# Performance work log

Hardware: AMD Instinct MI355X
Metric: run time of the kernel (lower is better)

Reference implementation:

```python
import jax, jax.numpy as jnp
import numpy as np

M_USERS = 100000
N_ITEMS = 50000
NUM_NODES = M_USERS + N_ITEMS
DIM = 64
N_EDGES = 3200000
BATCH = 1024
N_NEGS = 40
REG = 1e-4
NUM_LAYERS = 2


def setup_inputs() -> dict:
    key = jax.random.key(0)
    ks = jax.random.split(key, 14)
    xav = lambda k, shp: jax.random.normal(k, shp, dtype=jnp.float32) * np.float32(np.sqrt(2.0 / (shp[0] + shp[-1])))
    return {
        "E": xav(ks[0], (NUM_NODES, DIM)),
        "E2": xav(ks[1], (NUM_NODES, DIM)),
        "W0": xav(ks[2], (DIM, DIM)),
        "b0": jnp.zeros((DIM,), jnp.float32),
        "W1": xav(ks[3], (DIM, DIM)),
        "b1": jnp.zeros((DIM,), jnp.float32),
        "attn_W": xav(ks[4], (DIM, DIM)),
        "attn_b": jnp.zeros((DIM,), jnp.float32),
        "q_W": xav(ks[5], (1, DIM)),
        "w": jax.random.normal(ks[6], (BATCH,), dtype=jnp.float32),
        "edge_index": jax.random.randint(ks[7], (2, N_EDGES), 0, NUM_NODES, dtype=jnp.int64),
        "u": jax.random.randint(ks[8], (BATCH,), 0, M_USERS, dtype=jnp.int64),
        "v": jax.random.randint(ks[9], (BATCH,), 0, NUM_NODES, dtype=jnp.int64),
        "n": jax.random.randint(ks[10], (BATCH, N_NEGS), 0, NUM_NODES, dtype=jnp.int64),
    }


def _aggregate(E, E2, W0, b0, W1, b1, attn_W, attn_b, q_W, row, col):
    # LightGCN branch: symmetric degree-normalized scatter-add, NUM_LAYERS hops
    deg = jax.ops.segment_sum(jnp.ones_like(col, dtype=E.dtype), col, num_segments=NUM_NODES)
    dinv = jnp.where(deg > 0, jax.lax.rsqrt(jnp.maximum(deg, 1e-12)), 0.0)
    norm = dinv[row] * dinv[col]  # [E]

    def conv(x):
        msg = norm[:, None] * x[row]  # [E, D]
        return jax.ops.segment_sum(msg, col, num_segments=NUM_NODES)

    acc = E
    x = E
    for _ in range(NUM_LAYERS):
        x = conv(x)
        acc = acc + x
    z_p = acc / (NUM_LAYERS + 1)

    # MLP branch (eval mode: dropout disabled)
    h = jax.nn.relu(E2 @ W0.T + b0)
    z_n = jax.nn.relu(h @ W1.T + b1)

    # attention fusion
    w_p = jnp.tanh(z_p @ attn_W.T + attn_b) @ q_W.T  # [NUM_NODES, 1]
    w_n = jnp.tanh(z_n @ attn_W.T + attn_b) @ q_W.T
    alpha = jax.nn.softmax(jnp.concatenate([w_p, w_n], axis=1), axis=1)
    return alpha[:, :1] * z_p + alpha[:, 1:] * z_n


def reference(E, E2, W0, b0, W1, b1, attn_W, attn_b, q_W, w, edge_index, u, v, n):
    row, col = edge_index[0], edge_index[1]
    Z = _aggregate(E, E2, W0, b0, W1, b1, attn_W, attn_b, q_W, row, col)
    u_ = Z[u]            # [B, D]
    v_ = Z[v]            # [B, D]
    n_ = Z[n]            # [B, K, D]
    pos = jnp.sum(u_ * v_, axis=1)                      # [B]
    neg = jnp.einsum('bd,bkd->bk', u_, n_)              # [B, K]
    coef = -0.5 * jnp.sign(w) + 1.5                     # [B]
    sbpr = jax.nn.log_sigmoid(coef[:, None] * pos[:, None] - neg)  # [B, K]
    reg_loss = jnp.sum(u_ ** 2) + jnp.sum(v_ ** 2) + jnp.sum(n_ ** 2)
    return -jnp.sum(sbpr) + REG * reg_loss
```

## Files before the change

### kernel.cpp

```cpp
#include <hip/hip_runtime.h>
#include <hip/hip_fp8.h>
#include <math.h>

#define NUM_NODES 150000
#define DIM 64
#define N_EDGES 3200000
#define BATCH 1024
#define N_NEGS 40
#define REG_COEF 1e-4f

#define BK_BITS 9
#define BK_NODES 512
#define NBK ((NUM_NODES + BK_NODES - 1) >> BK_BITS)
#define TILE 8192
#define NT ((N_EDGES + TILE - 1) / TILE)
#define HSIZE (NBK * NT)
#define SCAN_B 1024
#define NB2 ((HSIZE + SCAN_B - 1) / SCAN_B)
#define NLIST (BATCH * (N_NEGS + 2))

typedef _Float16 half2v __attribute__((ext_vector_type(2)));
typedef _Float16 half4v __attribute__((ext_vector_type(4)));

__global__ __launch_bounds__(256) void histo_kernel(const int* __restrict__ col,
                                                    int* __restrict__ hist) {
    __shared__ int h[NBK];
    int t = threadIdx.x;
    for (int i = t; i < NBK; i += 256) h[i] = 0;
    __syncthreads();
    int e0 = blockIdx.x * TILE;
    int e1 = e0 + TILE; if (e1 > N_EDGES) e1 = N_EDGES;
    for (int i = e0 + t; i < e1; i += 256) atomicAdd(&h[col[i] >> BK_BITS], 1);
    __syncthreads();
    for (int i = t; i < NBK; i += 256) hist[i * NT + blockIdx.x] = h[i];
}

__global__ void scan_partial_kernel(const int* __restrict__ src, int* __restrict__ partial, int n) {
    int t = threadIdx.x;
    int g = blockIdx.x * SCAN_B + t;
    int v = (g < n) ? src[g] : 0;
    for (int m = 1; m < 64; m <<= 1) v += __shfl_xor(v, m);
    __shared__ int ws[16];
    if ((t & 63) == 0) ws[t >> 6] = v;
    __syncthreads();
    if (t < 16) {
        int s = ws[t];
        for (int m = 1; m < 16; m <<= 1) s += __shfl_xor(s, m);
        if (t == 0) partial[blockIdx.x] = s;
    }
}

__global__ void scan_base_kernel(int* __restrict__ partial, int nb, int chunks) {
    int l = threadIdx.x;
    int carry = 0;
    for (int c = 0; c < chunks; c++) {
        int idx = c * 64 + l;
        int v = (idx < nb) ? partial[idx] : 0;
        int inc = v;
        for (int m = 1; m < 64; m <<= 1) {
            int t = __shfl_up(inc, m);
            if (l >= m) inc += t;
        }
        int excl = inc - v + carry;
        if (idx < nb) partial[idx] = excl;
        carry += __shfl(inc, 63);
    }
}

__global__ void scan_apply_kernel(int* __restrict__ data, const int* __restrict__ partial, int n) {
    __shared__ int lds[SCAN_B];
    int t = threadIdx.x;
    int g = blockIdx.x * SCAN_B + t;
    int v = (g < n) ? data[g] : 0;
    int val = v;
    lds[t] = val;
    __syncthreads();
    for (int o = 1; o < SCAN_B; o <<= 1) {
        int add = (t >= o) ? lds[t - o] : 0;
        __syncthreads();
        val += add;
        lds[t] = val;
        __syncthreads();
    }
    if (g < n) data[g] = partial[blockIdx.x] + val - v;
}

__global__ __launch_bounds__(256) void partition_kernel(const int* __restrict__ row,
                                                        const int* __restrict__ col,
                                                        const int* __restrict__ hist,
                                                        unsigned* __restrict__ staging) {
    __shared__ int base[NBK];
    __shared__ int cnt[NBK];
    int t = threadIdx.x;
    for (int i = t; i < NBK; i += 256) { base[i] = hist[i * NT + blockIdx.x]; cnt[i] = 0; }
    __syncthreads();
    int e0 = blockIdx.x * TILE;
    int e1 = e0 + TILE; if (e1 > N_EDGES) e1 = N_EDGES;
    for (int i = e0 + t; i < e1; i += 256) {
        int c = col[i];
        int b = c >> BK_BITS;
        int r = atomicAdd(&cnt[b], 1);
        staging[base[b] + r] = ((unsigned)(c & (BK_NODES - 1)) << 18) | (unsigned)row[i];
    }
}

__global__ __launch_bounds__(512) void fill3_kernel(const int* __restrict__ hist,
                                                    const unsigned* __restrict__ staging,
                                                    const float* __restrict__ E,
                                                    int* __restrict__ off,
                                                    float* __restrict__ dinv,
                                                    float* __restrict__ sq,
                                                    int* __restrict__ csr_row,
                                                    __hip_fp8x4_e4m3* __restrict__ xnE4) {
    __shared__ int cnt[BK_NODES];
    __shared__ int lds[BK_NODES];
    __shared__ float sdinv[BK_NODES];
    int b = blockIdx.x;
    int t = threadIdx.x;
    int node0 = b << BK_BITS;
    int bstart = hist[b * NT];
    int bend = (b + 1 < NBK) ? hist[(b + 1) * NT] : N_EDGES;
    cnt[t] = 0;
    __syncthreads();
    for (int i = bstart + t; i < bend; i += 512) atomicAdd(&cnt[staging[i] >> 18], 1);
    __syncthreads();
    int v = cnt[t];
    int val = v;
    lds[t] = val;
    __syncthreads();
    for (int o = 1; o < BK_NODES; o <<= 1) {
        int add = (t >= o) ? lds[t - o] : 0;
        __syncthreads();
        val += add;
        lds[t] = val;
        __syncthreads();
    }
    int cursor = bstart + val - v;
    int node = node0 + t;
    float dv = (v > 0) ? rsqrtf((float)v) : 0.f;
    if (node < NUM_NODES) {
        off[node] = cursor;
        dinv[node] = dv;
        sq[node] = sqrtf((float)v);
    }
    sdinv[t] = dv;
    cnt[t] = cursor;
    __syncthreads();
    for (int i = bstart + t; i < bend; i += 512) {
        unsigned s = staging[i];
        int pos = atomicAdd(&cnt[s >> 18], 1);
        csr_row[pos] = (int)(s & 0x3FFFFu);
    }
    int nvalid = NUM_NODES - node0; if (nvalid > BK_NODES) nvalid = BK_NODES;
    int groups = nvalid << 4;
    const float4* E4 = (const float4*)E + ((size_t)node0 << 4);
    __hip_fp8x4_e4m3* out4 = xnE4 + ((size_t)node0 << 4);
    for (int gi = t; gi < groups; gi += 512) {
        float4 e = E4[gi];
        float s = 16.f * sdinv[gi >> 4];
        out4[gi] = __hip_fp8x4_e4m3(make_float4(s * e.x, s * e.y, s * e.z, s * e.w));
    }
    if (b == 0 && t == 0) off[NUM_NODES] = N_EDGES;
}

__global__ void flag_kernel(const int* __restrict__ u, const int* __restrict__ v,
                            const int* __restrict__ n, char* __restrict__ flags) {
    int i = blockIdx.x * blockDim.x + threadIdx.x;
    if (i >= NLIST) return;
    int id;
    if (i < BATCH) id = u[i];
    else if (i < 2 * BATCH) id = v[i - BATCH];
    else id = n[i - 2 * BATCH];
    flags[id] = 1;
}

__global__ void compact_kernel(const char* __restrict__ flags, int* __restrict__ list,
                               int* __restrict__ count) {
    int i = blockIdx.x * blockDim.x + threadIdx.x;
    if (i < NUM_NODES && flags[i]) {
        int pos = atomicAdd(count, 1);
        list[pos] = i;
    }
}

__global__ __launch_bounds__(256) void conv1_kernel(const int* __restrict__ off,
                                                    const int* __restrict__ csr_row,
                                                    const float* __restrict__ dinv,
                                                    const __hip_fp8x4_e4m3* __restrict__ xq,
                                                    _Float16* __restrict__ yh) {
    int gid = blockIdx.x * blockDim.x + threadIdx.x;
    int grp = gid >> 4;
    int g = threadIdx.x & 15;
    if (grp >= NUM_NODES) return;
    int start = off[grp];
    int end = off[grp + 1];
    float a0 = 0.f, a1 = 0.f, a2 = 0.f, a3 = 0.f;
    int i = start;
    for (; i + 3 < end; i += 4) {
        int r0 = csr_row[i];
        int r1 = csr_row[i + 1];
        int r2 = csr_row[i + 2];
        int r3 = csr_row[i + 3];
        float4 v0 = static_cast<float4>(xq[((size_t)r0 << 4) + g]);
        float4 v1 = static_cast<float4>(xq[((size_t)r1 << 4) + g]);
        float4 v2 = static_cast<float4>(xq[((size_t)r2 << 4) + g]);
        float4 v3 = static_cast<float4>(xq[((size_t)r3 << 4) + g]);
        a0 += v0.x + v1.x + v2.x + v3.x;
        a1 += v0.y + v1.y + v2.y + v3.y;
        a2 += v0.z + v1.z + v2.z + v3.z;
        a3 += v0.w + v1.w + v2.w + v3.w;
    }
    for (; i < end; ++i) {
        int r = csr_row[i];
        float4 v = static_cast<float4>(xq[((size_t)r << 4) + g]);
        a0 += v.x; a1 += v.y; a2 += v.z; a3 += v.w;
    }
    float dv = dinv[grp];
    float s = dv * dv * (1.f / 16.f);
    union { _Float16 h[4]; short4 s4; } u;
    u.h[0] = (_Float16)(s * a0);
    u.h[1] = (_Float16)(s * a1);
    u.h[2] = (_Float16)(s * a2);
    u.h[3] = (_Float16)(s * a3);
    ((short4*)yh)[((size_t)grp << 4) + g] = u.s4;
}

__global__ __launch_bounds__(256) void conv2_kernel(const int* __restrict__ off,
                                                    const int* __restrict__ csr_row,
                                                    const float* __restrict__ dinv,
                                                    const _Float16* __restrict__ xh,
                                                    float* __restrict__ x2,
                                                    const int* __restrict__ list,
                                                    const int* __restrict__ count) {
    int gid = blockIdx.x * blockDim.x + threadIdx.x;
    int li = gid >> 4;
    int g = threadIdx.x & 15;
    if (li >= *count) return;
    int nd = list[li];
    int start = off[nd];
    int end = off[nd + 1];
    const short4* xh4 = (const short4*)xh;
    float a0 = 0.f, a1 = 0.f, a2 = 0.f, a3 = 0.f;
    int i = start;
    for (; i + 3 < end; i += 4) {
        int r0 = csr_row[i];
        int r1 = csr_row[i + 1];
        int r2 = csr_row[i + 2];
        int r3 = csr_row[i + 3];
        union { short4 s4; _Float16 h[4]; } u0, u1, u2, u3;
        u0.s4 = xh4[((size_t)r0 << 4) + g];
        u1.s4 = xh4[((size_t)r1 << 4) + g];
        u2.s4 = xh4[((size_t)r2 << 4) + g];
        u3.s4 = xh4[((size_t)r3 << 4) + g];
        a0 += (float)u0.h[0] + (float)u1.h[0] + (float)u2.h[0] + (float)u3.h[0];
        a1 += (float)u0.h[1] + (float)u1.h[1] + (float)u2.h[1] + (float)u3.h[1];
        a2 += (float)u0.h[2] + (float)u1.h[2] + (float)u2.h[2] + (float)u3.h[2];
        a3 += (float)u0.h[3] + (float)u1.h[3] + (float)u2.h[3] + (float)u3.h[3];
    }
    for (; i < end; ++i) {
        int r = csr_row[i];
        union { short4 s4; _Float16 h[4]; } u;
        u.s4 = xh4[((size_t)r << 4) + g];
        a0 += (float)u.h[0]; a1 += (float)u.h[1];
        a2 += (float)u.h[2]; a3 += (float)u.h[3];
    }
    float dv = dinv[nd];
    ((float4*)x2)[((size_t)nd << 4) + g] = make_float4(dv * a0, dv * a1, dv * a2, dv * a3);
}

__global__ __launch_bounds__(256, 5) void fuse_kernel(
    const float* __restrict__ E, const float* __restrict__ E2,
    const float* __restrict__ W0, const float* __restrict__ b0,
    const float* __restrict__ W1, const float* __restrict__ b1,
    const float* __restrict__ AW, const float* __restrict__ ab,
    const float* __restrict__ qW,
    const _Float16* __restrict__ xn1, const float* __restrict__ sq,
    const float* x2, float* Z,
    const int* __restrict__ list, const int* __restrict__ count) {
    __shared__ __align__(16) _Float16 W0h[4096];
    __shared__ __align__(16) _Float16 W1h[4096];
    __shared__ __align__(16) _Float16 AWh[4096];
    __shared__ float bb0[64], bb1[64], bab[64], qb[64];
    __shared__ __align__(16) _Float16 xb[4][64];
    __shared__ __align__(16) _Float16 hb[4][64];
    __shared__ __align__(16) _Float16 zpb[4][64];
    __shared__ __align__(16) _Float16 znb[4][64];

    int t = threadIdx.x;
    for (int idx = t; idx < 4096; idx += 256) {
        int j = idx >> 6, k = idx & 63;
        int dst = (k >> 2) * 256 + j * 4 + (k & 3);
        W0h[dst] = (_Float16)W0[idx];
        W1h[dst] = (_Float16)W1[idx];
        AWh[dst] = (_Float16)AW[idx];
    }
    if (t < 64) { bb0[t] = b0[t]; bb1[t] = b1[t]; bab[t] = ab[t]; qb[t] = qW[t]; }
    __syncthreads();

    const int lane = t & 63, w = t >> 6;
    const int cnt = *count;
    const int stride = gridDim.x * 4;
    int li = blockIdx.x * 4 + w;

    int ndA = 0; float eA = 0.f, e2A = 0.f, x2A = 0.f, sqA = 0.f; _Float16 xnA = (_Float16)0.f;
    if (li < cnt) {
        ndA = list[li];
        size_t bA = ((size_t)ndA << 6) + lane;
        eA = E[bA]; e2A = E2[bA]; xnA = xn1[bA]; x2A = x2[bA]; sqA = sq[ndA];
    }

    for (; li < cnt; li += stride) {
        int liB = li + stride;
        int ndB = 0; float eB = 0.f, e2B = 0.f, x2B = 0.f, sqB = 0.f; _Float16 xnB = (_Float16)0.f;
        if (liB < cnt) {
            ndB = list[liB];
            size_t bB = ((size_t)ndB << 6) + lane;
            eB = E[bB]; e2B = E2[bB]; xnB = xn1[bB]; x2B = x2[bB]; sqB = sq[ndB];
        }

        size_t base = ((size_t)ndA << 6) + lane;
        float x1v = sqA * (float)xnA;
        float zp = (eA + x1v + x2A) * (1.f / 3.f);
        zpb[w][lane] = (_Float16)zp;
        xb[w][lane] = (_Float16)e2A;
        __builtin_amdgcn_wave_barrier();

        float s0 = bb0[lane], s1 = 0.f;
#pragma unroll
        for (int k4 = 0; k4 < 16; k4++) {
            half4v w4 = *(const half4v*)&W0h[k4 * 256 + lane * 4];
            half4v x4 = *(const half4v*)&xb[w][k4 * 4];
            s0 = __builtin_amdgcn_fdot2((half2v){w4.x, w4.y}, (half2v){x4.x, x4.y}, s0, false);
            s1 = __builtin_amdgcn_fdot2((half2v){w4.z, w4.w}, (half2v){x4.z, x4.w}, s1, false);
        }
        float h = fmaxf(s0 + s1, 0.f);
        hb[w][lane] = (_Float16)h;
        __builtin_amdgcn_wave_barrier();

        s0 = bb1[lane]; s1 = 0.f;
#pragma unroll
        for (int k4 = 0; k4 < 16; k4++) {
            half4v w4 = *(const half4v*)&W1h[k4 * 256 + lane * 4];
            half4v x4 = *(const half4v*)&hb[w][k4 * 4];
            s0 = __builtin_amdgcn_fdot2((half2v){w4.x, w4.y}, (half2v){x4.x, x4.y}, s0, false);
            s1 = __builtin_amdgcn_fdot2((half2v){w4.z, w4.w}, (half2v){x4.z, x4.w}, s1, false);
        }
        float zn = fmaxf(s0 + s1, 0.f);
        znb[w][lane] = (_Float16)zn;
        __builtin_amdgcn_wave_barrier();

        float sp0 = bab[lane], sp1 = 0.f, sn0 = 0.f, sn1 = 0.f;
#pragma unroll
        for (int k4 = 0; k4 < 16; k4++) {
            half4v w4 = *(const half4v*)&AWh[k4 * 256 + lane * 4];
            half4v p4 = *(const half4v*)&zpb[w][k4 * 4];
            half4v n4 = *(const half4v*)&znb[w][k4 * 4];
            sp0 = __builtin_amdgcn_fdot2((half2v){w4.x, w4.y}, (half2v){p4.x, p4.y}, sp0, false);
            sp1 = __builtin_amdgcn_fdot2((half2v){w4.z, w4.w}, (half2v){p4.z, p4.w}, sp1, false);
            sn0 = __builtin_amdgcn_fdot2((half2v){w4.x, w4.y}, (half2v){n4.x, n4.y}, sn0, false);
            sn1 = __builtin_amdgcn_fdot2((half2v){w4.z, w4.w}, (half2v){n4.z, n4.w}, sn1, false);
        }
        float tp = tanhf(sp0 + sp1) * qb[lane];
        float tn = tanhf(bab[lane] + sn0 + sn1) * qb[lane];
        for (int m = 1; m < 64; m <<= 1) {
            tp += __shfl_xor(tp, m);
            tn += __shfl_xor(tn, m);
        }
        float mx = fmaxf(tp, tn);
        float ep = expf(tp - mx), en = expf(tn - mx);
        float inv = 1.f / (ep + en);
        Z[base] = (ep * zp + en * zn) * inv;
        __builtin_amdgcn_wave_barrier();

        ndA = ndB; eA = eB; e2A = e2B; xnA = xnB; x2A = x2B; sqA = sqB;
    }
}

__global__ __launch_bounds__(256) void loss_kernel(const float* __restrict__ Z,
                                                   const float* __restrict__ wv,
                                                   const int* __restrict__ u,
                                                   const int* __restrict__ v,
                                                   const int* __restrict__ n,
                                                   float* __restrict__ out) {
    int wid = (blockIdx.x * blockDim.x + threadIdx.x) >> 6;
    int lane = threadIdx.x & 63;
    if (wid >= BATCH) return;
    float uu = Z[(size_t)u[wid] * DIM + lane];
    float vv = Z[(size_t)v[wid] * DIM + lane];
    float pos = uu * vv;
    for (int m = 1; m < 64; m <<= 1) pos += __shfl_xor(pos, m);
    float reg = uu * uu + vv * vv;
    float wval = wv[wid];
    float sgn = (wval > 0.f ? 1.f : 0.f) - (wval < 0.f ? 1.f : 0.f);
    float coef = -0.5f * sgn + 1.5f;
    float cp = coef * pos;
    float sb = 0.f;
    for (int k = 0; k < N_NEGS; k++) {
        int nid = n[wid * N_NEGS + k];
        float nn = Z[(size_t)nid * DIM + lane];
        float d = uu * nn;
        for (int m = 1; m < 64; m <<= 1) d += __shfl_xor(d, m);
        reg += nn * nn;
        float x = cp - d;
        float ls = (x >= 0.f) ? -log1pf(expf(-x)) : (x - log1pf(expf(x)));
        sb += ls;
    }
    for (int m = 1; m < 64; m <<= 1) reg += __shfl_xor(reg, m);
    if (lane == 0) atomicAdd(out, -sb + REG_COEF * reg);
}

extern "C" void kernel_launch(void* const* d_in, const int* in_sizes, int n_in,
                              void* d_out, int out_size, void* d_ws, size_t ws_size,
                              hipStream_t stream) {
    const float* E  = (const float*)d_in[0];
    const float* E2 = (const float*)d_in[1];
    const float* W0 = (const float*)d_in[2];
    const float* b0 = (const float*)d_in[3];
    const float* W1 = (const float*)d_in[4];
    const float* b1 = (const float*)d_in[5];
    const float* AW = (const float*)d_in[6];
    const float* ab = (const float*)d_in[7];
    const float* qW = (const float*)d_in[8];
    const float* wv = (const float*)d_in[9];
    const int* ei   = (const int*)d_in[10];
    const int* uu   = (const int*)d_in[11];
    const int* vv   = (const int*)d_in[12];
    const int* nn   = (const int*)d_in[13];
    const int* row = ei;
    const int* col = ei + N_EDGES;

    char* ws = (char*)d_ws;
    size_t p = 0;
    auto align_up = [](size_t x) { return (x + 255) & ~(size_t)255; };
    int* off        = (int*)(ws + p); p = align_up(p + (size_t)(NUM_NODES + 1) * 4);
    float* dinv     = (float*)(ws + p); p = align_up(p + (size_t)NUM_NODES * 4);
    float* sq       = (float*)(ws + p); p = align_up(p + (size_t)NUM_NODES * 4);
    int* hist       = (int*)(ws + p); p = align_up(p + (size_t)HSIZE * 4);
    int* partial    = (int*)(ws + p); p = align_up(p + (size_t)NB2 * 4);
    int* csr_row    = (int*)(ws + p); p = align_up(p + (size_t)N_EDGES * 4);
    char* flags     = (char*)(ws + p); p = align_up(p + (size_t)NUM_NODES);
    int* list       = (int*)(ws + p); p = align_up(p + (size_t)NLIST * 4);
    int* count      = (int*)(ws + p); p = align_up(p + 4);
    __hip_fp8x4_e4m3* xnE4 = (__hip_fp8x4_e4m3*)(ws + p); p = align_up(p + (size_t)NUM_NODES * DIM);
    _Float16* xn1   = (_Float16*)(ws + p); p = align_up(p + (size_t)NUM_NODES * DIM * 2);
    float* x2f      = (float*)(ws + p); p = align_up(p + (size_t)NUM_NODES * DIM * 4);
    float* Z = x2f;
    unsigned* staging = (unsigned*)x2f;

    hipMemsetAsync(d_out, 0, sizeof(float), stream);
    hipMemsetAsync(flags, 0, (size_t)NUM_NODES, stream);
    hipMemsetAsync(count, 0, 4, stream);

    histo_kernel<<<NT, 256, 0, stream>>>(col, hist);
    scan_partial_kernel<<<NB2, SCAN_B, 0, stream>>>(hist, partial, HSIZE);
    scan_base_kernel<<<1, 64, 0, stream>>>(partial, NB2, 2);
    scan_apply_kernel<<<NB2, SCAN_B, 0, stream>>>(hist, partial, HSIZE);
    partition_kernel<<<NT, 256, 0, stream>>>(row, col, hist, staging);
    fill3_kernel<<<NBK, 512, 0, stream>>>(hist, staging, E, off, dinv, sq, csr_row, xnE4);

    flag_kernel<<<(NLIST + 255) / 256, 256, 0, stream>>>(uu, vv, nn, flags);
    compact_kernel<<<(NUM_NODES + 255) / 256, 256, 0, stream>>>(flags, list, count);

    conv1_kernel<<<(NUM_NODES * 16 + 255) / 256, 256, 0, stream>>>(off, csr_row, dinv, xnE4, xn1);
    conv2_kernel<<<(NLIST * 16 + 255) / 256, 256, 0, stream>>>(off, csr_row, dinv, xn1, x2f, list, count);

    fuse_kernel<<<1280, 256, 0, stream>>>(E, E2, W0, b0, W1, b1, AW, ab, qW,
                                          xn1, sq, x2f, Z, list, count);

    loss_kernel<<<BATCH * 64 / 256, 256, 0, stream>>>(Z, wv, uu, vv, nn, (float*)d_out);
}
```

Measured before the change: 296.1 us.

## Build sorted node list via prefix scan instead of atomic compaction

Replaces the atomic-append compaction of flagged nodes with an int flag array, a three-pass prefix scan and an emit kernel, so the list of needed nodes comes out sorted by node id. This gives better locality for the later gathers and removes the contended atomic counter, at the cost of three extra kernel launches and a larger flag buffer. It also lowers the fuse kernel occupancy hint from 5 to 4 and simplifies its prefetch by clamping the next index rather than branching.

New measurement: 270.5 us. 1.09x faster.

```diff
diff --git a/kernel.cpp b/kernel.cpp
--- a/kernel.cpp
+++ b/kernel.cpp
@@ -17,6 +17,7 @@
 #define HSIZE (NBK * NT)
 #define SCAN_B 1024
 #define NB2 ((HSIZE + SCAN_B - 1) / SCAN_B)
+#define NB3 ((NUM_NODES + SCAN_B - 1) / SCAN_B)
 #define NLIST (BATCH * (N_NEGS + 2))
 
 typedef _Float16 half2v __attribute__((ext_vector_type(2)));
@@ -85,6 +86,25 @@
     if (g < n) data[g] = partial[blockIdx.x] + val - v;
 }
 
+__global__ void scan_apply2_kernel(const int* __restrict__ src, int* __restrict__ dst,
+                                   const int* __restrict__ partial, int n) {
+    __shared__ int lds[SCAN_B];
+    int t = threadIdx.x;
+    int g = blockIdx.x * SCAN_B + t;
+    int v = (g < n) ? src[g] : 0;
+    int val = v;
+    lds[t] = val;
+    __syncthreads();
+    for (int o = 1; o < SCAN_B; o <<= 1) {
+        int add = (t >= o) ? lds[t - o] : 0;
+        __syncthreads();
+        val += add;
+        lds[t] = val;
+        __syncthreads();
+    }
+    if (g < n) dst[g] = partial[blockIdx.x] + val - v;
+}
+
 __global__ __launch_bounds__(256) void partition_kernel(const int* __restrict__ row,
                                                         const int* __restrict__ col,
                                                         const int* __restrict__ hist,
@@ -164,7 +184,7 @@
 }
 
 __global__ void flag_kernel(const int* __restrict__ u, const int* __restrict__ v,
-                            const int* __restrict__ n, char* __restrict__ flags) {
+                            const int* __restrict__ n, int* __restrict__ flags) {
     int i = blockIdx.x * blockDim.x + threadIdx.x;
     if (i >= NLIST) return;
     int id;
@@ -174,13 +194,12 @@
     flags[id] = 1;
 }
 
-__global__ void compact_kernel(const char* __restrict__ flags, int* __restrict__ list,
-                               int* __restrict__ count) {
+__global__ void emit_list_kernel(const int* __restrict__ flags, const int* __restrict__ posb,
+                                 int* __restrict__ list, int* __restrict__ count) {
     int i = blockIdx.x * blockDim.x + threadIdx.x;
-    if (i < NUM_NODES && flags[i]) {
-        int pos = atomicAdd(count, 1);
-        list[pos] = i;
-    }
+    if (i >= NUM_NODES) return;
+    if (flags[i]) list[posb[i]] = i;
+    if (i == NUM_NODES - 1) *count = posb[i] + flags[i];
 }
 
 __global__ __launch_bounds__(256) void conv1_kernel(const int* __restrict__ off,
@@ -268,7 +287,7 @@
     ((float4*)x2)[((size_t)nd << 4) + g] = make_float4(dv * a0, dv * a1, dv * a2, dv * a3);
 }
 
-__global__ __launch_bounds__(256, 5) void fuse_kernel(
+__global__ __launch_bounds__(256, 4) void fuse_kernel(
     const float* __restrict__ E, const float* __restrict__ E2,
     const float* __restrict__ W0, const float* __restrict__ b0,
     const float* __restrict__ W1, const float* __restrict__ b1,
@@ -301,22 +320,21 @@
     const int cnt = *count;
     const int stride = gridDim.x * 4;
     int li = blockIdx.x * 4 + w;
-
-    int ndA = 0; float eA = 0.f, e2A = 0.f, x2A = 0.f, sqA = 0.f; _Float16 xnA = (_Float16)0.f;
-    if (li < cnt) {
-        ndA = list[li];
-        size_t bA = ((size_t)ndA << 6) + lane;
-        eA = E[bA]; e2A = E2[bA]; xnA = xn1[bA]; x2A = x2[bA]; sqA = sq[ndA];
-    }
+    if (li >= cnt) return;
+
+    int ndA = list[li];
+    {
+    }
+    size_t bA0 = ((size_t)ndA << 6) + lane;
+    float eA = E[bA0], e2A = E2[bA0], x2A = x2[bA0], sqA = sq[ndA];
+    _Float16 xnA = xn1[bA0];
 
     for (; li < cnt; li += stride) {
-        int liB = li + stride;
-        int ndB = 0; float eB = 0.f, e2B = 0.f, x2B = 0.f, sqB = 0.f; _Float16 xnB = (_Float16)0.f;
-        if (liB < cnt) {
-            ndB = list[liB];
-            size_t bB = ((size_t)ndB << 6) + lane;
-            eB = E[bB]; e2B = E2[bB]; xnB = xn1[bB]; x2B = x2[bB]; sqB = sq[ndB];
-        }
+        int liB = li + stride; liB = (liB < cnt) ? liB : (cnt - 1);
+        int ndB = list[liB];
+        size_t bB = ((size_t)ndB << 6) + lane;
+        float eB = E[bB], e2B = E2[bB], x2B = x2[bB], sqB = sq[ndB];
+        _Float16 xnB = xn1[bB];
 
         size_t base = ((size_t)ndA << 6) + lane;
         float x1v = sqA * (float)xnA;
@@ -438,7 +456,8 @@
     int* hist       = (int*)(ws + p); p = align_up(p + (size_t)HSIZE * 4);
     int* partial    = (int*)(ws + p); p = align_up(p + (size_t)NB2 * 4);
     int* csr_row    = (int*)(ws + p); p = align_up(p + (size_t)N_EDGES * 4);
-    char* flags     = (char*)(ws + p); p = align_up(p + (size_t)NUM_NODES);
+    int* flagi      = (int*)(ws + p); p = align_up(p + (size_t)NUM_NODES * 4);
+    int* posb       = (int*)(ws + p); p = align_up(p + (size_t)NUM_NODES * 4);
     int* list       = (int*)(ws + p); p = align_up(p + (size_t)NLIST * 4);
     int* count      = (int*)(ws + p); p = align_up(p + 4);
     __hip_fp8x4_e4m3* xnE4 = (__hip_fp8x4_e4m3*)(ws + p); p = align_up(p + (size_t)NUM_NODES * DIM);
@@ -448,8 +467,7 @@
     unsigned* staging = (unsigned*)x2f;
 
     hipMemsetAsync(d_out, 0, sizeof(float), stream);
-    hipMemsetAsync(flags, 0, (size_t)NUM_NODES, stream);
-    hipMemsetAsync(count, 0, 4, stream);
+    hipMemsetAsync(flagi, 0, (size_t)NUM_NODES * 4, stream);
 
     histo_kernel<<<NT, 256, 0, stream>>>(col, hist);
     scan_partial_kernel<<<NB2, SCAN_B, 0, stream>>>(hist, partial, HSIZE);
@@ -458,8 +476,11 @@
     partition_kernel<<<NT, 256, 0, stream>>>(row, col, hist, staging);
     fill3_kernel<<<NBK, 512, 0, stream>>>(hist, staging, E, off, dinv, sq, csr_row, xnE4);
 
-    flag_kernel<<<(NLIST + 255) / 256, 256, 0, stream>>>(uu, vv, nn, flags);
-    compact_kernel<<<(NUM_NODES + 255) / 256, 256, 0, stream>>>(flags, list, count);
+    flag_kernel<<<(NLIST + 255) / 256, 256, 0, stream>>>(uu, vv, nn, flagi);
+    scan_partial_kernel<<<NB3, SCAN_B, 0, stream>>>(flagi, partial, NUM_NODES);
+    scan_base_kernel<<<1, 64, 0, stream>>>(partial, NB3, 3);
+    scan_apply2_kernel<<<NB3, SCAN_B, 0, stream>>>(flagi, posb, partial, NUM_NODES);
+    emit_list_kernel<<<(NUM_NODES + 255) / 256, 256, 0, stream>>>(flagi, posb, list, count);
 
     conv1_kernel<<<(NUM_NODES * 16 + 255) / 256, 256, 0, stream>>>(off, csr_row, dinv, xnE4, xn1);
     conv2_kernel<<<(NLIST * 16 + 255) / 256, 256, 0, stream>>>(off, csr_row, dinv, xn1, x2f, list, count);
```
